# Optimization experiments

Measured on AMD Instinct MI355X. Metric: run time of the kernel, lower is better.

The kernel has to match this reference:

```python
import jax, jax.numpy as jnp
import numpy as np

DIM = 512

def setup_inputs() -> dict:
    key = jax.random.key(0)
    k1, k2, k3 = jax.random.split(key, 3)
    x = jax.random.normal(k1, (4, DIM, 64, 64), dtype=jnp.float32)
    w1 = jax.random.normal(k2, (DIM, DIM), dtype=jnp.float32) * (DIM ** -0.5)
    w2 = jax.random.normal(k3, (DIM, DIM), dtype=jnp.float32) * (DIM ** -0.5)
    return {"x": x, "w1": w1, "w2": w2}

def reference(x, w1, w2):
    b, c, h, w = x.shape
    scale = c ** -0.5
    # [b, n, c] with n = h*w spatial tokens
    f = x.reshape(b, c, h * w).transpose(0, 2, 1)
    q = jnp.einsum('bnc,dc->bnd', f, w1)          # linear1 (no bias)
    attn = jnp.einsum('bnd,bmd->bnm', q, f) * scale
    attn = jax.nn.softmax(attn, axis=-1)
    v = jnp.einsum('bnc,dc->bnd', f, w2)          # linear2 (no bias)
    mixed = jnp.einsum('bnm,bmd->bnd', attn, v)
    return mixed.transpose(0, 2, 1).reshape(b, c, h, w)
```

## Files before the change

### kernel.cpp

```cpp
#include <hip/hip_runtime.h>
#include <stdint.h>


typedef __attribute__((ext_vector_type(8)))  short          short8;
typedef __attribute__((ext_vector_type(4)))  float          f32x4;
typedef __attribute__((ext_vector_type(4)))  unsigned short u16x4;
typedef __attribute__((ext_vector_type(8)))  unsigned short u16x8;

#define N_TOK 4096
#define CDIM  512
#define NT    64
#define WSCALE (1.4426950408889634f * 0.04419417382415922f)

static __device__ __forceinline__ unsigned short f2bf(float f){
  unsigned int u = __builtin_bit_cast(unsigned int, f);
  u += 0x7fffu + ((u >> 16) & 1u);
  return (unsigned short)(u >> 16);
}
static __device__ __forceinline__ unsigned int pk2bf(float a, float b){
  unsigned int ua = __builtin_bit_cast(unsigned int, a);
  ua += 0x7fffu + ((ua >> 16) & 1u);
  unsigned int ub = __builtin_bit_cast(unsigned int, b);
  ub += 0x7fffu + ((ub >> 16) & 1u);
  return (ua >> 16) | (ub & 0xffff0000u);
}
static __device__ __forceinline__ void gl_lds16(const void* g, void* l){
  __builtin_amdgcn_global_load_lds((__attribute__((address_space(1))) void*)g,
                                   (__attribute__((address_space(3))) void*)l,
                                   16, 0, 0);
}

__global__ void k_castw(const float* __restrict__ w1, const float* __restrict__ w2,
                        unsigned short* __restrict__ w1b, unsigned short* __restrict__ w2b){
  int i = blockIdx.x * 256 + threadIdx.x;
  float4 a = ((const float4*)w1)[i];
  float4 c = ((const float4*)w2)[i];
  u16x4 oa = { f2bf(a.x*WSCALE), f2bf(a.y*WSCALE), f2bf(a.z*WSCALE), f2bf(a.w*WSCALE) };
  u16x4 oc = { f2bf(c.x), f2bf(c.y), f2bf(c.z), f2bf(c.w) };
  *(u16x4*)(w1b + (size_t)i*4) = oa;
  *(u16x4*)(w2b + (size_t)i*4) = oc;
}

__global__ void k_transpose(const float* __restrict__ x, unsigned short* __restrict__ Kb){
  __shared__ float tile[64][65];
  const int b = blockIdx.z, c0 = blockIdx.y*64, n0 = blockIdx.x*64;
  const int t = threadIdx.x;
#pragma unroll
  for(int i=0;i<4;i++){
    int flat = i*256 + t;
    int row = flat>>4, ch = flat&15;
    float4 v = *(const float4*)(x + ((size_t)(b*CDIM + c0 + row))*N_TOK + n0 + ch*4);
    tile[row][ch*4+0]=v.x; tile[row][ch*4+1]=v.y; tile[row][ch*4+2]=v.z; tile[row][ch*4+3]=v.w;
  }
  __syncthreads();
#pragma unroll
  for(int i=0;i<2;i++){
    int flat = i*256 + t;
    int nr = flat>>3, cc = flat&7;
    u16x8 o;
#pragma unroll
    for(int e=0;e<8;e++) o[e] = f2bf(tile[cc*8+e][nr]);
    *(u16x8*)(Kb + ((size_t)b*N_TOK + n0 + nr)*CDIM + c0 + cc*8) = o;
  }
}

__global__ __launch_bounds__(256, 2)
void k_gemm_bt(const unsigned short* __restrict__ A, const unsigned short* __restrict__ B,
               unsigned short* __restrict__ C,
               long Abstride, long Bbstride, long Cbstride, int ldc)
{
  __shared__ unsigned short Asm[128*32];
  __shared__ unsigned short Bsm[128*32];
  const int b = blockIdx.z;
  const unsigned short* Ab = A + (size_t)b*Abstride;
  const unsigned short* Bb = B + (size_t)b*Bbstride;
  unsigned short* Cb = C + (size_t)b*Cbstride;
  const int t = threadIdx.x, w = t>>6, lane = t&63;
  const int wr = w>>1, wc = w&1;
  const size_t am0 = (size_t)blockIdx.x*128;
  const size_t bn0 = (size_t)blockIdx.y*128;

  f32x4 acc[4][4];
#pragma unroll
  for(int i=0;i<4;i++)
#pragma unroll
    for(int j=0;j<4;j++)
#pragma unroll
      for(int r=0;r<4;r++) acc[i][j][r]=0.f;

  for(int k0=0;k0<CDIM;k0+=32){
#pragma unroll
    for(int i=0;i<2;i++){
      int flat = i*256 + t;
      int row = flat>>2, ch = flat&3;
      gl_lds16(Ab + (am0+row)*CDIM + k0 + ch*8, &Asm[(size_t)(i*256 + w*64)*8]);
    }
#pragma unroll
    for(int i=0;i<2;i++){
      int flat = i*256 + t;
      int row = flat>>2, ch = flat&3;
      gl_lds16(Bb + (bn0+row)*CDIM + k0 + ch*8, &Bsm[(size_t)(i*256 + w*64)*8]);
    }
    __syncthreads();
    short8 af[4], bfr[4];
#pragma unroll
    for(int i=0;i<4;i++){
      af[i]  = *(const short8*)&Asm[(wr*64 + i*16 + (lane&15))*32 + (lane>>4)*8];
      bfr[i] = *(const short8*)&Bsm[(wc*64 + i*16 + (lane&15))*32 + (lane>>4)*8];
    }
#pragma unroll
    for(int i=0;i<4;i++)
#pragma unroll
      for(int j=0;j<4;j++)
        acc[i][j] = __builtin_amdgcn_mfma_f32_16x16x32_bf16(af[i], bfr[j], acc[i][j], 0,0,0);
    __syncthreads();
  }
#pragma unroll
  for(int i=0;i<4;i++)
#pragma unroll
    for(int j=0;j<4;j++){
      size_t m0 = am0 + wr*64 + i*16 + (lane>>4)*4;
      size_t n  = bn0 + wc*64 + j*16 + (lane&15);
#pragma unroll
      for(int r=0;r<4;r++)
        Cb[(m0+r)*(size_t)ldc + n] = f2bf(acc[i][j][r]);
    }
}

__global__ __launch_bounds__(512, 1)
void k_attn(const unsigned short* __restrict__ Qb, const unsigned short* __restrict__ Kb,
            const unsigned short* __restrict__ Vt,
            float* __restrict__ Op0, float* __restrict__ Op1,
            float* __restrict__ Lp)
{
  __shared__ unsigned short Ks[2][32*512];
  __shared__ unsigned short Vs[2][512*32];
  const int nb = blockIdx.x, b = blockIdx.y, kvh = blockIdx.z;
  const int t = threadIdx.x, w = t>>6, lane = t&63;
  const int g = lane>>4, q15 = lane&15;
  const int qrow = nb*128 + w*16 + q15;
  const size_t bK = (size_t)b*N_TOK*CDIM;
  const size_t bV = (size_t)b*CDIM*N_TOK;
  const int kvbase = kvh*2048;

  short8 qreg[16];
  {
    const unsigned short* qp = Qb + bK + (size_t)qrow*CDIM + g*8;
#pragma unroll
    for(int cs=0;cs<16;cs++) qreg[cs] = *(const short8*)(qp + cs*32);
  }

  f32x4 accO[32];
#pragma unroll
  for(int dt=0;dt<32;dt++)
#pragma unroll
    for(int r=0;r<4;r++) accO[dt][r]=0.f;

  float lsum = 0.f;

  auto stage = [&](int kt, int bb){
    const int kv0 = kvbase + kt*32;
#pragma unroll
    for(int j=0;j<4;j++){
      int r = w*4 + j;
      gl_lds16(Kb + bK + (size_t)(kv0+r)*CDIM + ((lane ^ (r&7))*8),
               &Ks[bb][(size_t)r*512]);
    }
#pragma unroll
    for(int j=0;j<4;j++){
      int base = (w*4+j)*64;
      int flat = base + lane;
      int d = flat>>2, c4 = flat&3;
      gl_lds16(Vt + bV + (size_t)d*N_TOK + kv0 + ((c4 ^ ((d>>2)&3))*8),
               &Vs[bb][(size_t)base*8]);
    }
  };

  stage(0, 0);
  __syncthreads();

  for(int kt=0; kt<NT; ++kt){
    const int cur = kt&1;
    if(kt<NT-1) stage(kt+1, cur^1);

    const unsigned short* ksb = &Ks[cur][0];
    f32x4 s0, s1;
#pragma unroll
    for(int r=0;r<4;r++){ s0[r]=0.f; s1[r]=0.f; }
    __builtin_amdgcn_s_setprio(1);
#pragma unroll
    for(int cs=0;cs<16;cs++){
      int slot = (cs*4 + g) ^ (q15&7);
      short8 a0 = *(const short8*)(ksb + (size_t)q15*512      + slot*8);
      short8 a1 = *(const short8*)(ksb + (size_t)(16+q15)*512 + slot*8);
      s0 = __builtin_amdgcn_mfma_f32_16x16x32_bf16(a0, qreg[cs], s0, 0,0,0);
      s1 = __builtin_amdgcn_mfma_f32_16x16x32_bf16(a1, qreg[cs], s1, 0,0,0);
    }
    __builtin_amdgcn_s_setprio(0);

    float z[8];
#pragma unroll
    for(int r=0;r<4;r++){ z[r] = exp2f(s0[r]); z[4+r] = exp2f(s1[r]); }
    float ps = z[0]+z[1]+z[2]+z[3]+z[4]+z[5]+z[6]+z[7];
    ps += __shfl_xor(ps, 16);
    ps += __shfl_xor(ps, 32);
    lsum += ps;

    {
      int w0 = (int)pk2bf(z[0], z[1]);
      int w1 = (int)pk2bf(z[2], z[3]);
      int w2 = (int)pk2bf(z[4], z[5]);
      int w3 = (int)pk2bf(z[6], z[7]);
      int srcA = (q15 + ((g&1)<<5)) << 2;
      int srcB = srcA + (16<<2);
      int A00 = __builtin_amdgcn_ds_bpermute(srcA, w0);
      int A01 = __builtin_amdgcn_ds_bpermute(srcA, w1);
      int A10 = __builtin_amdgcn_ds_bpermute(srcA, w2);
      int A11 = __builtin_amdgcn_ds_bpermute(srcA, w3);
      int B00 = __builtin_amdgcn_ds_bpermute(srcB, w0);
      int B01 = __builtin_amdgcn_ds_bpermute(srcB, w1);
      int B10 = __builtin_amdgcn_ds_bpermute(srcB, w2);
      int B11 = __builtin_amdgcn_ds_bpermute(srcB, w3);
      const bool tt = (g>>1) != 0;
      union { int u[4]; short8 v; } pu;
      pu.u[0] = tt ? A10 : A00;
      pu.u[1] = tt ? A11 : A01;
      pu.u[2] = tt ? B10 : B00;
      pu.u[3] = tt ? B11 : B01;
      short8 pf = pu.v;

      const unsigned short* vsb = &Vs[cur][0];
      __builtin_amdgcn_s_setprio(1);
#pragma unroll
      for(int dt=0;dt<32;dt++){
        int vrow = dt*16 + q15;
        int slot = g ^ ((vrow>>2)&3);
        short8 vf = *(const short8*)(vsb + (size_t)vrow*32 + slot*8);
        accO[dt] = __builtin_amdgcn_mfma_f32_16x16x32_bf16(vf, pf, accO[dt], 0,0,0);
      }
      __builtin_amdgcn_s_setprio(0);
    }
    __syncthreads();
  }

  float* Op = kvh ? Op1 : Op0;
#pragma unroll
  for(int dt=0;dt<32;dt++)
#pragma unroll
    for(int r=0;r<4;r++){
      int d = dt*16 + 4*g + r;
      Op[bV + (size_t)d*N_TOK + qrow] = accO[dt][r];
    }
  if(g==0){
    int idx = kvh*16384 + b*4096 + qrow;
    Lp[idx] = lsum;
  }
}

__global__ void k_merge(const float* __restrict__ O1, const float* __restrict__ Lp,
                        float* __restrict__ out)
{
  size_t i4 = ((size_t)blockIdx.x*256 + threadIdx.x) * 4;
  int n = (int)(i4 & 4095);
  int b = (int)(i4 >> 21);
  float4 o0 = *(const float4*)(out + i4);
  float4 o1 = *(const float4*)(O1 + i4);
  float4 l0 = *(const float4*)(Lp + b*4096 + n);
  float4 l1 = *(const float4*)(Lp + 16384 + b*4096 + n);
  float4 r;
#pragma unroll
  for(int e=0;e<4;e++){
    float num = ((const float*)&o0)[e] + ((const float*)&o1)[e];
    float den = ((const float*)&l0)[e] + ((const float*)&l1)[e];
    ((float*)&r)[e] = num / den;
  }
  *(float4*)(out + i4) = r;
}

extern "C" void kernel_launch(void* const* d_in, const int* in_sizes, int n_in,
                              void* d_out, int out_size, void* d_ws, size_t ws_size,
                              hipStream_t stream)
{
  const float* x  = (const float*)d_in[0];
  const float* w1 = (const float*)d_in[1];
  const float* w2 = (const float*)d_in[2];
  float* out = (float*)d_out;

  unsigned short* ws  = (unsigned short*)d_ws;
  unsigned short* w1b = ws;
  unsigned short* w2b = ws + 262144;
  unsigned short* Kb  = ws + 524288;
  unsigned short* Qb  = Kb + (size_t)4*N_TOK*CDIM;
  unsigned short* Vtb = Qb + (size_t)4*N_TOK*CDIM;
  float* O1f = (float*)(Vtb + (size_t)4*N_TOK*CDIM);
  float* Lpf = O1f + (size_t)4*CDIM*N_TOK;

  k_castw    <<<256, 256, 0, stream>>>(w1, w2, w1b, w2b);
  k_transpose<<<dim3(64,8,4), 256, 0, stream>>>(x, Kb);
  k_gemm_bt  <<<dim3(32,4,4), 256, 0, stream>>>(Kb, w1b, Qb,
              (long)N_TOK*CDIM, 0L, (long)N_TOK*CDIM, CDIM);
  k_gemm_bt  <<<dim3(4,32,4), 256, 0, stream>>>(w2b, Kb, Vtb,
              0L, (long)N_TOK*CDIM, (long)CDIM*N_TOK, N_TOK);
  k_attn     <<<dim3(32,4,2), 512, 0, stream>>>(Qb, Kb, Vtb, out, O1f, Lpf);
  k_merge    <<<8192, 256, 0, stream>>>(O1f, Lpf, out);
}
```

Before: 290.7 us.

## Split attention KV into four chunks with single-buffered blocks at occupancy two

Adds a new attention kernel that splits the key/value range into four chunks instead of two, doubling the grid to 512 blocks. It uses single-buffered shared memory and asks for two blocks per CU, so loads can overlap across blocks instead of through double buffering. A four-way merge kernel combines the partial outputs and sums. This targets under-filled CUs (256 blocks on a 256-CU part), at the cost of more partial-output traffic, possible register spilling under the tighter launch bound, and a fallback path that depends on workspace size.

```diff
diff --git a/kernel.cpp b/kernel.cpp
--- a/kernel.cpp
+++ b/kernel.cpp
@@ -9,7 +9,6 @@
 
 #define N_TOK 4096
 #define CDIM  512
-#define NT    64
 #define WSCALE (1.4426950408889634f * 0.04419417382415922f)
 
 static __device__ __forceinline__ unsigned short f2bf(float f){
@@ -127,11 +126,132 @@
     }
 }
 
+static __device__ __forceinline__ void attn_tile_compute(
+    const unsigned short* ksb, const unsigned short* vsb,
+    const short8* qreg, f32x4* accO, float& lsum, int g, int q15)
+{
+  f32x4 s0, s1;
+#pragma unroll
+  for(int r=0;r<4;r++){ s0[r]=0.f; s1[r]=0.f; }
+  __builtin_amdgcn_s_setprio(1);
+#pragma unroll
+  for(int cs=0;cs<16;cs++){
+    int slot = (cs*4 + g) ^ (q15&7);
+    short8 a0 = *(const short8*)(ksb + (size_t)q15*512      + slot*8);
+    short8 a1 = *(const short8*)(ksb + (size_t)(16+q15)*512 + slot*8);
+    s0 = __builtin_amdgcn_mfma_f32_16x16x32_bf16(a0, qreg[cs], s0, 0,0,0);
+    s1 = __builtin_amdgcn_mfma_f32_16x16x32_bf16(a1, qreg[cs], s1, 0,0,0);
+  }
+  __builtin_amdgcn_s_setprio(0);
+
+  float z[8];
+#pragma unroll
+  for(int r=0;r<4;r++){ z[r] = exp2f(s0[r]); z[4+r] = exp2f(s1[r]); }
+  float ps = z[0]+z[1]+z[2]+z[3]+z[4]+z[5]+z[6]+z[7];
+  ps += __shfl_xor(ps, 16);
+  ps += __shfl_xor(ps, 32);
+  lsum += ps;
+
+  int w0 = (int)pk2bf(z[0], z[1]);
+  int w1 = (int)pk2bf(z[2], z[3]);
+  int w2 = (int)pk2bf(z[4], z[5]);
+  int w3 = (int)pk2bf(z[6], z[7]);
+  int srcA = (q15 + ((g&1)<<5)) << 2;
+  int srcB = srcA + (16<<2);
+  int A00 = __builtin_amdgcn_ds_bpermute(srcA, w0);
+  int A01 = __builtin_amdgcn_ds_bpermute(srcA, w1);
+  int A10 = __builtin_amdgcn_ds_bpermute(srcA, w2);
+  int A11 = __builtin_amdgcn_ds_bpermute(srcA, w3);
+  int B00 = __builtin_amdgcn_ds_bpermute(srcB, w0);
+  int B01 = __builtin_amdgcn_ds_bpermute(srcB, w1);
+  int B10 = __builtin_amdgcn_ds_bpermute(srcB, w2);
+  int B11 = __builtin_amdgcn_ds_bpermute(srcB, w3);
+  const bool tt = (g>>1) != 0;
+  union { int u[4]; short8 v; } pu;
+  pu.u[0] = tt ? A10 : A00;
+  pu.u[1] = tt ? A11 : A01;
+  pu.u[2] = tt ? B10 : B00;
+  pu.u[3] = tt ? B11 : B01;
+  short8 pf = pu.v;
+
+  __builtin_amdgcn_s_setprio(1);
+#pragma unroll
+  for(int dt=0;dt<32;dt++){
+    int vrow = dt*16 + q15;
+    int slot = g ^ ((vrow>>2)&3);
+    short8 vf = *(const short8*)(vsb + (size_t)vrow*32 + slot*8);
+    accO[dt] = __builtin_amdgcn_mfma_f32_16x16x32_bf16(vf, pf, accO[dt], 0,0,0);
+  }
+  __builtin_amdgcn_s_setprio(0);
+}
+
+__global__ __launch_bounds__(512, 2)
+void k_attn_sb(const unsigned short* __restrict__ Qb, const unsigned short* __restrict__ Kb,
+               const unsigned short* __restrict__ Vt,
+               float* __restrict__ Op0, float* __restrict__ Op1,
+               float* __restrict__ Op2, float* __restrict__ Op3,
+               float* __restrict__ Lp)
+{
+  __shared__ unsigned short Ks[32*512];
+  __shared__ unsigned short Vs[512*32];
+  const int nb = blockIdx.x, b = blockIdx.y, kvh = blockIdx.z;
+  const int t = threadIdx.x, w = t>>6, lane = t&63;
+  const int g = lane>>4, q15 = lane&15;
+  const int qrow = nb*128 + w*16 + q15;
+  const size_t bK = (size_t)b*N_TOK*CDIM;
+  const size_t bV = (size_t)b*CDIM*N_TOK;
+  const int kvbase = kvh*1024;
+
+  short8 qreg[16];
+  {
+    const unsigned short* qp = Qb + bK + (size_t)qrow*CDIM + g*8;
+#pragma unroll
+    for(int cs=0;cs<16;cs++) qreg[cs] = *(const short8*)(qp + cs*32);
+  }
+  f32x4 accO[32];
+#pragma unroll
+  for(int dt=0;dt<32;dt++)
+#pragma unroll
+    for(int r=0;r<4;r++) accO[dt][r]=0.f;
+  float lsum = 0.f;
+
+  for(int kt=0; kt<32; ++kt){
+    const int kv0 = kvbase + kt*32;
+#pragma unroll
+    for(int j=0;j<4;j++){
+      int r = w*4 + j;
+      gl_lds16(Kb + bK + (size_t)(kv0+r)*CDIM + ((lane ^ (r&7))*8),
+               &Ks[(size_t)r*512]);
+    }
+#pragma unroll
+    for(int j=0;j<4;j++){
+      int base = (w*4+j)*64;
+      int flat = base + lane;
+      int d = flat>>2, c4 = flat&3;
+      gl_lds16(Vt + bV + (size_t)d*N_TOK + kv0 + ((c4 ^ ((d>>2)&3))*8),
+               &Vs[(size_t)base*8]);
+    }
+    __syncthreads();
+    attn_tile_compute(&Ks[0], &Vs[0], qreg, accO, lsum, g, q15);
+    __syncthreads();
+  }
+
+  float* Op = (kvh==0)?Op0:(kvh==1)?Op1:(kvh==2)?Op2:Op3;
+#pragma unroll
+  for(int dt=0;dt<32;dt++)
+#pragma unroll
+    for(int r=0;r<4;r++){
+      int d = dt*16 + 4*g + r;
+      Op[bV + (size_t)d*N_TOK + qrow] = accO[dt][r];
+    }
+  if(g==0) Lp[kvh*16384 + b*4096 + qrow] = lsum;
+}
+
 __global__ __launch_bounds__(512, 1)
-void k_attn(const unsigned short* __restrict__ Qb, const unsigned short* __restrict__ Kb,
-            const unsigned short* __restrict__ Vt,
-            float* __restrict__ Op0, float* __restrict__ Op1,
-            float* __restrict__ Lp)
+void k_attn_db(const unsigned short* __restrict__ Qb, const unsigned short* __restrict__ Kb,
+               const unsigned short* __restrict__ Vt,
+               float* __restrict__ Op0, float* __restrict__ Op1,
+               float* __restrict__ Lp)
 {
   __shared__ unsigned short Ks[2][32*512];
   __shared__ unsigned short Vs[2][512*32];
@@ -149,13 +269,11 @@
 #pragma unroll
     for(int cs=0;cs<16;cs++) qreg[cs] = *(const short8*)(qp + cs*32);
   }
-
   f32x4 accO[32];
 #pragma unroll
   for(int dt=0;dt<32;dt++)
 #pragma unroll
     for(int r=0;r<4;r++) accO[dt][r]=0.f;
-
   float lsum = 0.f;
 
   auto stage = [&](int kt, int bb){
@@ -178,68 +296,10 @@
 
   stage(0, 0);
   __syncthreads();
-
-  for(int kt=0; kt<NT; ++kt){
+  for(int kt=0; kt<64; ++kt){
     const int cur = kt&1;
-    if(kt<NT-1) stage(kt+1, cur^1);
-
-    const unsigned short* ksb = &Ks[cur][0];
-    f32x4 s0, s1;
-#pragma unroll
-    for(int r=0;r<4;r++){ s0[r]=0.f; s1[r]=0.f; }
-    __builtin_amdgcn_s_setprio(1);
-#pragma unroll
-    for(int cs=0;cs<16;cs++){
-      int slot = (cs*4 + g) ^ (q15&7);
-      short8 a0 = *(const short8*)(ksb + (size_t)q15*512      + slot*8);
-      short8 a1 = *(const short8*)(ksb + (size_t)(16+q15)*512 + slot*8);
-      s0 = __builtin_amdgcn_mfma_f32_16x16x32_bf16(a0, qreg[cs], s0, 0,0,0);
-      s1 = __builtin_amdgcn_mfma_f32_16x16x32_bf16(a1, qreg[cs], s1, 0,0,0);
-    }
-    __builtin_amdgcn_s_setprio(0);
-
-    float z[8];
-#pragma unroll
-    for(int r=0;r<4;r++){ z[r] = exp2f(s0[r]); z[4+r] = exp2f(s1[r]); }
-    float ps = z[0]+z[1]+z[2]+z[3]+z[4]+z[5]+z[6]+z[7];
-    ps += __shfl_xor(ps, 16);
-    ps += __shfl_xor(ps, 32);
-    lsum += ps;
-
-    {
-      int w0 = (int)pk2bf(z[0], z[1]);
-      int w1 = (int)pk2bf(z[2], z[3]);
-      int w2 = (int)pk2bf(z[4], z[5]);
-      int w3 = (int)pk2bf(z[6], z[7]);
-      int srcA = (q15 + ((g&1)<<5)) << 2;
-      int srcB = srcA + (16<<2);
-      int A00 = __builtin_amdgcn_ds_bpermute(srcA, w0);
-      int A01 = __builtin_amdgcn_ds_bpermute(srcA, w1);
-      int A10 = __builtin_amdgcn_ds_bpermute(srcA, w2);
-      int A11 = __builtin_amdgcn_ds_bpermute(srcA, w3);
-      int B00 = __builtin_amdgcn_ds_bpermute(srcB, w0);
-      int B01 = __builtin_amdgcn_ds_bpermute(srcB, w1);
-      int B10 = __builtin_amdgcn_ds_bpermute(srcB, w2);
-      int B11 = __builtin_amdgcn_ds_bpermute(srcB, w3);
-      const bool tt = (g>>1) != 0;
-      union { int u[4]; short8 v; } pu;
-      pu.u[0] = tt ? A10 : A00;
-      pu.u[1] = tt ? A11 : A01;
-      pu.u[2] = tt ? B10 : B00;
-      pu.u[3] = tt ? B11 : B01;
-      short8 pf = pu.v;
-
-      const unsigned short* vsb = &Vs[cur][0];
-      __builtin_amdgcn_s_setprio(1);
-#pragma unroll
-      for(int dt=0;dt<32;dt++){
-        int vrow = dt*16 + q15;
-        int slot = g ^ ((vrow>>2)&3);
-        short8 vf = *(const short8*)(vsb + (size_t)vrow*32 + slot*8);
-        accO[dt] = __builtin_amdgcn_mfma_f32_16x16x32_bf16(vf, pf, accO[dt], 0,0,0);
-      }
-      __builtin_amdgcn_s_setprio(0);
-    }
+    if(kt<63) stage(kt+1, cur^1);
+    attn_tile_compute(&Ks[cur][0], &Vs[cur][0], qreg, accO, lsum, g, q15);
     __syncthreads();
   }
 
@@ -251,14 +311,38 @@
       int d = dt*16 + 4*g + r;
       Op[bV + (size_t)d*N_TOK + qrow] = accO[dt][r];
     }
-  if(g==0){
-    int idx = kvh*16384 + b*4096 + qrow;
-    Lp[idx] = lsum;
-  }
-}
-
-__global__ void k_merge(const float* __restrict__ O1, const float* __restrict__ Lp,
-                        float* __restrict__ out)
+  if(g==0) Lp[kvh*16384 + b*4096 + qrow] = lsum;
+}
+
+__global__ void k_merge4(const float* __restrict__ O1, const float* __restrict__ O2,
+                         const float* __restrict__ O3, const float* __restrict__ Lp,
+                         float* __restrict__ out)
+{
+  size_t i4 = ((size_t)blockIdx.x*256 + threadIdx.x) * 4;
+  int n = (int)(i4 & 4095);
+  int b = (int)(i4 >> 21);
+  float4 o0 = *(const float4*)(out + i4);
+  float4 o1 = *(const float4*)(O1 + i4);
+  float4 o2 = *(const float4*)(O2 + i4);
+  float4 o3 = *(const float4*)(O3 + i4);
+  float4 l0 = *(const float4*)(Lp +             b*4096 + n);
+  float4 l1 = *(const float4*)(Lp + 1*16384 + b*4096 + n);
+  float4 l2 = *(const float4*)(Lp + 2*16384 + b*4096 + n);
+  float4 l3 = *(const float4*)(Lp + 3*16384 + b*4096 + n);
+  float4 r;
+#pragma unroll
+  for(int e=0;e<4;e++){
+    float num = ((const float*)&o0)[e] + ((const float*)&o1)[e]
+              + ((const float*)&o2)[e] + ((const float*)&o3)[e];
+    float den = ((const float*)&l0)[e] + ((const float*)&l1)[e]
+              + ((const float*)&l2)[e] + ((const float*)&l3)[e];
+    ((float*)&r)[e] = num / den;
+  }
+  *(float4*)(out + i4) = r;
+}
+
+__global__ void k_merge2(const float* __restrict__ O1, const float* __restrict__ Lp,
+                         float* __restrict__ out)
 {
   size_t i4 = ((size_t)blockIdx.x*256 + threadIdx.x) * 4;
   int n = (int)(i4 & 4095);
@@ -293,7 +377,11 @@
   unsigned short* Qb  = Kb + (size_t)4*N_TOK*CDIM;
   unsigned short* Vtb = Qb + (size_t)4*N_TOK*CDIM;
   float* O1f = (float*)(Vtb + (size_t)4*N_TOK*CDIM);
-  float* Lpf = O1f + (size_t)4*CDIM*N_TOK;
+  const size_t OSZ = (size_t)4*CDIM*N_TOK;
+  float* O2f = O1f + OSZ;
+  float* O3f = O2f + OSZ;
+  float* Lpf4 = O3f + OSZ;
+  const size_t need4 = 51380224 + 3*OSZ*4 + 4*16384*4;
 
   k_castw    <<<256, 256, 0, stream>>>(w1, w2, w1b, w2b);
   k_transpose<<<dim3(64,8,4), 256, 0, stream>>>(x, Kb);
@@ -301,6 +389,13 @@
               (long)N_TOK*CDIM, 0L, (long)N_TOK*CDIM, CDIM);
   k_gemm_bt  <<<dim3(4,32,4), 256, 0, stream>>>(w2b, Kb, Vtb,
               0L, (long)N_TOK*CDIM, (long)CDIM*N_TOK, N_TOK);
-  k_attn     <<<dim3(32,4,2), 512, 0, stream>>>(Qb, Kb, Vtb, out, O1f, Lpf);
-  k_merge    <<<8192, 256, 0, stream>>>(O1f, Lpf, out);
-}
+
+  if (ws_size >= need4) {
+    k_attn_sb<<<dim3(32,4,4), 512, 0, stream>>>(Qb, Kb, Vtb, out, O1f, O2f, O3f, Lpf4);
+    k_merge4 <<<8192, 256, 0, stream>>>(O1f, O2f, O3f, Lpf4, out);
+  } else {
+    float* Lpf2 = O1f + OSZ;
+    k_attn_db<<<dim3(32,4,2), 512, 0, stream>>>(Qb, Kb, Vtb, out, O1f, Lpf2);
+    k_merge2 <<<8192, 256, 0, stream>>>(O1f, Lpf2, out);
+  }
+}
```

New measurement: 316.1 us. 8.7% more time.
